# Optimization experiments

Measured on AMD Instinct MI355X. Metric: run time of the kernel, lower is better.

The kernel has to match this reference:

```python
import jax, jax.numpy as jnp
import numpy as np

B, HW, N = 4, 65536, 48
NEAR, FAR = 0.1, 10.0


def setup_inputs() -> dict:
    key = jax.random.key(0)
    k1, k2, k3 = jax.random.split(key, 3)
    rgb = jax.random.uniform(k1, (B, HW, N, 3), dtype=jnp.float32)
    sigma = jax.random.uniform(k2, (B, HW, N, 1), dtype=jnp.float32)
    # sorted sample depths in [near, far] along each ray
    z = jax.random.uniform(k3, (B, HW, N), dtype=jnp.float32)
    z_vals = NEAR + (FAR - NEAR) * jnp.sort(z, axis=-1)
    return {"rgb": rgb, "sigma": sigma, "z_vals": z_vals}


def reference(rgb, sigma, z_vals):
    # distances between consecutive samples; last dist is a huge cap value
    dists = z_vals[..., 1:] - z_vals[..., :-1]                       # (B, HW, N-1)
    dists = jnp.concatenate(
        [dists, jnp.full_like(dists[..., :1], 1e10)], axis=-1)      # (B, HW, N)
    alpha = 1.0 - jnp.exp(-sigma[..., 0] * dists)                    # (B, HW, N)
    # transmittance: exclusive cumulative product of (1 - alpha)
    T = jnp.cumprod(1.0 - alpha + 1e-10, axis=-1)
    T = jnp.concatenate([jnp.ones_like(T[..., :1]), T[..., :-1]], axis=-1)
    weights = alpha * T                                              # (B, HW, N)
    rgb_map = jnp.einsum('bns,bnsc->bnc', weights, rgb)              # (B, HW, 3)
    depth_map = jnp.sum(weights * z_vals, axis=-1)                   # (B, HW)
    return rgb_map, depth_map
```

## Files before the change

kernel.cpp:

```cpp
#include <hip/hip_runtime.h>

#define N_SAMP 48
#define TPR 4
#define SPT (N_SAMP / TPR)
#define RPB 64
#define BLOCK (RPB * TPR)

__global__ __launch_bounds__(BLOCK) void volrender_kernel(
    const float4* __restrict__ rgb4,
    const float4* __restrict__ sigma4,
    const float4* __restrict__ z4,
    float* __restrict__ out_rgb,
    float* __restrict__ out_depth,
    int n_rays)
{
    const int t   = threadIdx.x;
    const int rl  = t >> 2;
    const int q   = t & 3;
    const int ray = blockIdx.x * RPB + rl;

    const int rayc = (ray < n_rays) ? ray : (n_rays - 1);

    float rloc[SPT * 3];
    float4* rv = reinterpret_cast<float4*>(rloc);
    {
        const size_t rb = (size_t)rayc * 36 + (size_t)q * 9;
#pragma unroll
        for (int k = 0; k < 9; ++k) rv[k] = rgb4[rb + k];
    }

    float zloc[SPT];
    float4* zv = reinterpret_cast<float4*>(zloc);
    float sloc[SPT];
    float4* sv = reinterpret_cast<float4*>(sloc);
    {
        const size_t zb = (size_t)rayc * 12 + (size_t)q * 3;
#pragma unroll
        for (int k = 0; k < 3; ++k) zv[k] = z4[zb + k];
#pragma unroll
        for (int k = 0; k < 3; ++k) sv[k] = sigma4[zb + k];
    }

    const int lane    = threadIdx.x & 63;
    const float znext = __shfl(zloc[0], (lane + 1) & 63);

    float T = 1.0f;
    float ar = 0.0f, ag = 0.0f, ab = 0.0f, ad = 0.0f;
#pragma unroll
    for (int j = 0; j < SPT; ++j) {
        const float zn   = (j < SPT - 1) ? zloc[j + 1] : znext;
        const bool  last = (j == SPT - 1);
        float dist  = (last && q == TPR - 1) ? 1e10f : (zn - zloc[j]);
        float alpha = 1.0f - __expf(-sloc[j] * dist);
        float w     = alpha * T;
        T *= (1.0f - alpha + 1e-10f);
        ar = fmaf(w, rloc[3 * j + 0], ar);
        ag = fmaf(w, rloc[3 * j + 1], ag);
        ab = fmaf(w, rloc[3 * j + 2], ab);
        ad = fmaf(w, zloc[j], ad);
    }

    const int  base = lane & ~3;
    const float P   = T;
    const float P0  = __shfl(P, base + 0);
    const float P1  = __shfl(P, base + 1);
    const float P2  = __shfl(P, base + 2);
    float Tpre = 1.0f;
    if (q > 0) Tpre *= P0;
    if (q > 1) Tpre *= P1;
    if (q > 2) Tpre *= P2;

    ar *= Tpre; ag *= Tpre; ab *= Tpre; ad *= Tpre;

    ar += __shfl_xor(ar, 1); ag += __shfl_xor(ag, 1);
    ab += __shfl_xor(ab, 1); ad += __shfl_xor(ad, 1);
    ar += __shfl_xor(ar, 2); ag += __shfl_xor(ag, 2);
    ab += __shfl_xor(ab, 2); ad += __shfl_xor(ad, 2);

    if (q == 0 && ray < n_rays) {
        out_rgb[(size_t)ray * 3 + 0] = ar;
        out_rgb[(size_t)ray * 3 + 1] = ag;
        out_rgb[(size_t)ray * 3 + 2] = ab;
        out_depth[ray] = ad;
    }
}

extern "C" void kernel_launch(void* const* d_in, const int* in_sizes, int n_in,
                              void* d_out, int out_size, void* d_ws, size_t ws_size,
                              hipStream_t stream) {
    const float4* rgb4   = (const float4*)d_in[0];
    const float4* sigma4 = (const float4*)d_in[1];
    const float4* z4     = (const float4*)d_in[2];

    const int n_rays = in_sizes[2] / N_SAMP;

    float* out_rgb   = (float*)d_out;
    float* out_depth = out_rgb + (size_t)n_rays * 3;

    const int grid = (n_rays + RPB - 1) / RPB;
    hipLaunchKernelGGL(volrender_kernel, dim3(grid), dim3(BLOCK), 0, stream,
                       rgb4, sigma4, z4, out_rgb, out_depth, n_rays);
}
```

Before: 280.6 us.

## Interleave sample chunks across ray threads for coalesced loads and shorter serial chains

Each of the four threads per ray now loads three interleaved 4-sample chunks instead of one contiguous 12-sample block. Adjacent lanes therefore read adjacent float4s, which should improve load coalescing. Each chunk's transmittance chain is computed on its own, giving three independent serial cumprod chains per thread that can overlap. The chunks are then combined with per-round shuffle prefix products across the four threads. The cost is more shuffles and more register state, and the bookkeeping for the next z sample across chunks is more complex.

```diff
diff --git a/kernel.cpp b/kernel.cpp
--- a/kernel.cpp
+++ b/kernel.cpp
@@ -2,7 +2,8 @@
 
 #define N_SAMP 48
 #define TPR 4
-#define SPT (N_SAMP / TPR)
+#define ROUNDS 3
+#define CSZ 4
 #define RPB 64
 #define BLOCK (RPB * TPR)
 
@@ -14,63 +15,86 @@
     float* __restrict__ out_depth,
     int n_rays)
 {
-    const int t   = threadIdx.x;
-    const int rl  = t >> 2;
-    const int q   = t & 3;
-    const int ray = blockIdx.x * RPB + rl;
-
+    const int t    = threadIdx.x;
+    const int rl   = t >> 2;
+    const int q    = t & 3;
+    const int ray  = blockIdx.x * RPB + rl;
     const int rayc = (ray < n_rays) ? ray : (n_rays - 1);
 
-    float rloc[SPT * 3];
-    float4* rv = reinterpret_cast<float4*>(rloc);
+    float zloc[ROUNDS][CSZ];
+    float sloc[ROUNDS][CSZ];
+    float rloc[ROUNDS][CSZ * 3];
+
     {
-        const size_t rb = (size_t)rayc * 36 + (size_t)q * 9;
+        const size_t zb = (size_t)rayc * 12 + q;
 #pragma unroll
-        for (int k = 0; k < 9; ++k) rv[k] = rgb4[rb + k];
+        for (int r = 0; r < ROUNDS; ++r)
+            *reinterpret_cast<float4*>(zloc[r]) = z4[zb + 4 * r];
+#pragma unroll
+        for (int r = 0; r < ROUNDS; ++r)
+            *reinterpret_cast<float4*>(sloc[r]) = sigma4[zb + 4 * r];
+        const size_t rb = (size_t)rayc * 36 + 3 * q;
+#pragma unroll
+        for (int r = 0; r < ROUNDS; ++r)
+#pragma unroll
+            for (int k = 0; k < 3; ++k)
+                reinterpret_cast<float4*>(rloc[r])[k] = rgb4[rb + 12 * r + k];
+    }
+    __builtin_amdgcn_sched_barrier(0);
+
+    const int lane = t & 63;
+    const int base = lane & ~3;
+
+    float A[ROUNDS];
+#pragma unroll
+    for (int r = 0; r < ROUNDS; ++r)
+        A[r] = __shfl(zloc[r][0], base + ((q + 1) & 3));
+
+    float Q[ROUNDS];
+    float car[ROUNDS], cag[ROUNDS], cab[ROUNDS], cad[ROUNDS];
+#pragma unroll
+    for (int r = 0; r < ROUNDS; ++r) {
+        const float znext = (q < 3) ? A[r] : A[(r < ROUNDS - 1) ? r + 1 : r];
+        float T = 1.0f, ar = 0.0f, ag = 0.0f, ab = 0.0f, ad = 0.0f;
+#pragma unroll
+        for (int j = 0; j < CSZ; ++j) {
+            const float zn   = (j < CSZ - 1) ? zloc[r][j + 1] : znext;
+            const bool  gl   = (r == ROUNDS - 1) && (q == TPR - 1) && (j == CSZ - 1);
+            const float dist = gl ? 1e10f : (zn - zloc[r][j]);
+            const float alpha = 1.0f - __expf(-sloc[r][j] * dist);
+            const float w     = alpha * T;
+            T *= (1.0f - alpha + 1e-10f);
+            ar = fmaf(w, rloc[r][3 * j + 0], ar);
+            ag = fmaf(w, rloc[r][3 * j + 1], ag);
+            ab = fmaf(w, rloc[r][3 * j + 2], ab);
+            ad = fmaf(w, zloc[r][j], ad);
+        }
+        Q[r] = T;
+        car[r] = ar; cag[r] = ag; cab[r] = ab; cad[r] = ad;
     }
 
-    float zloc[SPT];
-    float4* zv = reinterpret_cast<float4*>(zloc);
-    float sloc[SPT];
-    float4* sv = reinterpret_cast<float4*>(sloc);
-    {
-        const size_t zb = (size_t)rayc * 12 + (size_t)q * 3;
+    float pre[ROUNDS], R[ROUNDS];
 #pragma unroll
-        for (int k = 0; k < 3; ++k) zv[k] = z4[zb + k];
-#pragma unroll
-        for (int k = 0; k < 3; ++k) sv[k] = sigma4[zb + k];
+    for (int r = 0; r < ROUNDS; ++r) {
+        const float q0 = __shfl(Q[r], base + 0);
+        const float q1 = __shfl(Q[r], base + 1);
+        const float q2 = __shfl(Q[r], base + 2);
+        const float q3 = __shfl(Q[r], base + 3);
+        float p = 1.0f;
+        if (q > 0) p *= q0;
+        if (q > 1) p *= q1;
+        if (q > 2) p *= q2;
+        pre[r] = p;
+        R[r]   = q0 * q1 * q2 * q3;
     }
+    const float S0 = pre[0];
+    const float S1 = R[0] * pre[1];
+    const float S2 = R[0] * R[1] * pre[2];
 
-    const int lane    = threadIdx.x & 63;
-    const float znext = __shfl(zloc[0], (lane + 1) & 63);
-
-    float T = 1.0f;
-    float ar = 0.0f, ag = 0.0f, ab = 0.0f, ad = 0.0f;
-#pragma unroll
-    for (int j = 0; j < SPT; ++j) {
-        const float zn   = (j < SPT - 1) ? zloc[j + 1] : znext;
-        const bool  last = (j == SPT - 1);
-        float dist  = (last && q == TPR - 1) ? 1e10f : (zn - zloc[j]);
-        float alpha = 1.0f - __expf(-sloc[j] * dist);
-        float w     = alpha * T;
-        T *= (1.0f - alpha + 1e-10f);
-        ar = fmaf(w, rloc[3 * j + 0], ar);
-        ag = fmaf(w, rloc[3 * j + 1], ag);
-        ab = fmaf(w, rloc[3 * j + 2], ab);
-        ad = fmaf(w, zloc[j], ad);
-    }
-
-    const int  base = lane & ~3;
-    const float P   = T;
-    const float P0  = __shfl(P, base + 0);
-    const float P1  = __shfl(P, base + 1);
-    const float P2  = __shfl(P, base + 2);
-    float Tpre = 1.0f;
-    if (q > 0) Tpre *= P0;
-    if (q > 1) Tpre *= P1;
-    if (q > 2) Tpre *= P2;
-
-    ar *= Tpre; ag *= Tpre; ab *= Tpre; ad *= Tpre;
+    float ar = S0 * car[0]; ar = fmaf(S1, car[1], ar); ar = fmaf(S2, car[2], ar);
+    float ag = S0 * cag[0]; ag = fmaf(S1, cag[1], ag); ag = fmaf(S2, cag[2], ag);
+    float ab = S0 * cab[0]; ab = fmaf(S1, cab[1], ab); ab = fmaf(S2, cab[2], ab);
+    float ad = S0 * cad[0]; ad = fmaf(S1, cad[1], ad); ad = fmaf(S2, cad[2], ad);
 
     ar += __shfl_xor(ar, 1); ag += __shfl_xor(ag, 1);
     ab += __shfl_xor(ab, 1); ad += __shfl_xor(ad, 1);
```

After: 276.6 us. No clear change (-1.4%).
